# Kernel tuning notes

Hardware: AMD Instinct MI355X
Metric: run time of the kernel (lower is better)

The kernel has to match this reference:

```python
import jax, jax.numpy as jnp
import numpy as np

V, MAXLEN, D, I, C, L, S = 32000, 4096, 1024, 4096, 1024, 4, 4096


def setup_inputs() -> dict:
    key = jax.random.key(0)
    ks = jax.random.split(key, 20)
    sd = 0.02
    inp = {
        "input_indices": jax.random.randint(ks[0], (S,), 0, V),
        "emb": jax.random.normal(ks[1], (V, D), jnp.float32) * sd,
        "pos": jax.random.normal(ks[2], (MAXLEN, D), jnp.float32) * sd,
        "Wq": jax.random.normal(ks[3], (L, D, I), jnp.float32) * sd,
        "bq": jnp.zeros((L, I), jnp.float32),
        "Wk": jax.random.normal(ks[4], (L, D, I), jnp.float32) * sd,
        "bk": jnp.zeros((L, I), jnp.float32),
        "Wv": jax.random.normal(ks[5], (L, D, I), jnp.float32) * sd,
        "bv": jnp.zeros((L, I), jnp.float32),
        "Wo": jax.random.normal(ks[6], (L, I, D), jnp.float32) * sd,
        "bo": jnp.zeros((L, D), jnp.float32),
        "W1": jax.random.normal(ks[7], (L, D, I), jnp.float32) * sd,
        "b1": jnp.zeros((L, I), jnp.float32),
        "W2": jax.random.normal(ks[8], (L, I, D), jnp.float32) * sd,
        "b2": jnp.zeros((L, D), jnp.float32),
        "Wout": jax.random.normal(ks[9], (D, C), jnp.float32) * sd,
        "bout": jnp.zeros((C,), jnp.float32),
    }
    return inp


def reference(input_indices, emb, pos, Wq, bq, Wk, bk, Wv, bv, Wo, bo, W1, b1, W2, b2, Wout, bout):
    s = input_indices.shape[0]
    x = emb[input_indices] + pos[:s]  # [S, D]
    causal_mask = jnp.triu(jnp.ones((s, s), bool), k=1)  # True above diagonal -> masked
    scale = 1.0 / np.sqrt(Wq.shape[-1]).astype(np.float32)

    def layer(x, p):
        wq, bq_, wk, bk_, wv, bv_, wo, bo_, w1, b1_, w2, b2_ = p
        q = x @ wq + bq_  # [S, I]
        k = x @ wk + bk_
        v = x @ wv + bv_
        scores = (q @ k.T) * scale  # [S, S]
        scores = jnp.where(causal_mask, -jnp.inf, scores)
        attn = jax.nn.softmax(scores, axis=-1)
        r = x + (attn @ v) @ wo + bo_  # residual + attention output projection
        f = jnp.maximum(r @ w1 + b1_, 0.0) @ w2 + b2_  # ReLU FFN
        return r + f, attn

    x, attention_maps = jax.lax.scan(
        layer, x, (Wq, bq, Wk, bk, Wv, bv, Wo, bo, W1, b1, W2, b2)
    )
    logits = x @ Wout + bout  # [S, C]
    log_probs = jax.nn.log_softmax(logits, axis=-1)
    return log_probs, attention_maps  # [S, C], [L, S, S]
```

## Files before the change

kernel.cpp:

```cpp
#include <hip/hip_runtime.h>
#include <stdint.h>
#include <math.h>

#define S_ 4096
#define D_ 1024
#define I_ 4096
#define C_ 1024
#define L_ 4

typedef unsigned short u16;
typedef short bf16x8 __attribute__((ext_vector_type(8)));
typedef float f32x4 __attribute__((ext_vector_type(4)));

__device__ __forceinline__ u16 f2bf(float f) {
  union { float f; uint32_t u; } c; c.f = f;
  return (u16)((c.u + 0x7FFFu + ((c.u >> 16) & 1u)) >> 16);
}

__device__ __forceinline__ u16 f2h(float f) {
  _Float16 h = (_Float16)f;
  return *(u16*)&h;
}
__device__ __forceinline__ float h2f(u16 b) {
  _Float16 h = *(_Float16*)&b;
  return (float)h;
}

__device__ __forceinline__ void gll16(const void* g, void* l) {
  __builtin_amdgcn_global_load_lds(
      (__attribute__((address_space(1))) void*)(g),
      (__attribute__((address_space(3))) void*)(l), 16, 0, 0);
}

#define BAR() asm volatile("s_barrier" ::: "memory")
#define WAITV(n) asm volatile("s_waitcnt vmcnt(" #n ")" ::: "memory")

__device__ __forceinline__ int xcd_swz(int orig, int nwg) {
  int q8 = nwg >> 3, r8 = nwg & 7;
  int xcd = orig & 7, rem = orig >> 3;
  return (xcd < r8 ? xcd * (q8 + 1) : r8 * (q8 + 1) + (xcd - r8) * q8) + rem;
}

__device__ __forceinline__ void gemm256_body(
    u16* sA, u16* sB,
    const u16* __restrict__ A, const u16* __restrict__ Bt,
    const float* __restrict__ bias, const float* __restrict__ resid,
    float* __restrict__ outF, u16* __restrict__ outB, u16* __restrict__ outH,
    u16* __restrict__ outT, int ldT,
    int N, int K, float scale, int relu,
    int row0, int col0, int t0, int t1)
{
  int tid = threadIdx.x, l = tid & 63;
  int w = tid >> 6;
  int wr = w >> 2, wc = w & 3;
  int lrow = l & 15, lq = l >> 4;
  int hb = wc >> 1;
  int rx = lrow & 7;

  const u16* ap[2]; const u16* bp[2]; int dst[2];
#pragma unroll
  for (int u = 0; u < 2; ++u) {
    int c = u * 512 + tid;
    int row = c >> 3;
    int oct = (c & 7) ^ (row & 7);
    ap[u] = A + (size_t)(row0 + row) * K + oct * 8;
    bp[u] = Bt + (size_t)(col0 + row) * K + oct * 8;
    dst[u] = c * 8;
  }

#define STAGE_A(par, hh, t)                                                     \
  { _Pragma("unroll") for (int u = 0; u < 2; ++u)                               \
      gll16(ap[u] + (size_t)(hh) * 128 * K + (t) * 64,                          \
            &sA[((par) * 2 + (hh)) * 8192 + dst[u]]); }
#define STAGE_B(par, hh, t)                                                     \
  { _Pragma("unroll") for (int u = 0; u < 2; ++u)                               \
      gll16(bp[u] + (size_t)(hh) * 128 * K + (t) * 64,                          \
            &sB[((par) * 2 + (hh)) * 8192 + dst[u]]); }
#define LD_A(DST, par, mh)                                                      \
  { _Pragma("unroll") for (int mi = 0; mi < 4; ++mi)                            \
    _Pragma("unroll") for (int kc = 0; kc < 2; ++kc)                            \
      DST[mi][kc] = *(const bf16x8*)&sA[((par) * 2 + wr) * 8192 +               \
          ((mh) * 64 + mi * 16 + lrow) * 64 + (((kc * 4 + lq) ^ rx) * 8)]; }
#define LD_B(DST, par, nh)                                                      \
  { _Pragma("unroll") for (int nj = 0; nj < 2; ++nj)                            \
    _Pragma("unroll") for (int kc = 0; kc < 2; ++kc)                            \
      DST[nj][kc] = *(const bf16x8*)&sB[((par) * 2 + hb) * 8192 +               \
          ((wc & 1) * 64 + (nh) * 32 + nj * 16 + lrow) * 64 +                   \
          (((kc * 4 + lq) ^ rx) * 8)]; }

  f32x4 acc[8][4];
#pragma unroll
  for (int i = 0; i < 8; ++i)
#pragma unroll
    for (int j = 0; j < 4; ++j) {
      acc[i][j][0] = 0.f; acc[i][j][1] = 0.f; acc[i][j][2] = 0.f; acc[i][j][3] = 0.f;
    }

#define MM(AF, MB, NB)                                                          \
  { __builtin_amdgcn_s_setprio(1);                                             \
    _Pragma("unroll") for (int kc = 0; kc < 2; ++kc)                            \
    _Pragma("unroll") for (int mi = 0; mi < 4; ++mi)                            \
    _Pragma("unroll") for (int nj = 0; nj < 2; ++nj)                            \
      acc[(MB) + mi][(NB) + nj] = __builtin_amdgcn_mfma_f32_16x16x32_bf16(      \
          AF[mi][kc], bfv[nj][kc], acc[(MB) + mi][(NB) + nj], 0, 0, 0);         \
    __builtin_amdgcn_s_setprio(0); }

  bf16x8 afA[4][2], afB[4][2], bfv[2][2];

  STAGE_A(0, 0, t0); STAGE_A(0, 1, t0); STAGE_B(0, 0, t0); STAGE_B(0, 1, t0);
  STAGE_A(1, 0, t0 + 1); STAGE_A(1, 1, t0 + 1); STAGE_B(1, 0, t0 + 1);
  WAITV(6);
  BAR();

  for (int t = t0; t < t1; ++t) {
    int p = (t - t0) & 1;
    LD_A(afA, p, 0);
    LD_B(bfv, p, 0);
    LD_A(afB, p, 1);
    if (t + 1 < t1) STAGE_B(p ^ 1, 1, t + 1);
    BAR();
    MM(afA, 0, 0);
    BAR();
    if (t + 2 < t1) STAGE_A(p, 0, t + 2);
    BAR();
    MM(afB, 4, 0);
    BAR();
    LD_B(bfv, p, 1);
    if (t + 2 < t1) STAGE_A(p, 1, t + 2);
    BAR();
    MM(afB, 4, 2);
    BAR();
    if (t + 2 < t1) STAGE_B(p, 0, t + 2);
    BAR();
    MM(afA, 0, 2);
    if (t + 2 < t1) { WAITV(6); } else { WAITV(0); }
    BAR();
  }
#undef STAGE_A
#undef STAGE_B
#undef LD_A
#undef LD_B
#undef MM

  float biasv[4] = {0.f, 0.f, 0.f, 0.f};
  if (bias) {
#pragma unroll
    for (int j = 0; j < 4; ++j) biasv[j] = bias[col0 + wc * 64 + j * 16 + lrow];
  }

  if (outT) {
    u16* tlds = sA;
    int myhalf = wc >> 1;
    int colb = tid >> 5;
    int sub = tid & 31;
#pragma unroll
    for (int half = 0; half < 2; ++half) {
      BAR();
      if (myhalf == half) {
#pragma unroll
        for (int i = 0; i < 8; ++i)
#pragma unroll
          for (int r = 0; r < 4; ++r)
#pragma unroll
            for (int j = 0; j < 4; ++j) {
              int cl = (wc * 64 + j * 16 + lrow) & 127;
              int rowl = wr * 128 + i * 16 + lq * 4 + r;
              tlds[cl * 264 + rowl] = f2bf(acc[i][j][r] + biasv[j]);
            }
      }
      BAR();
#pragma unroll
      for (int it = 0; it < 8; ++it) {
        int cl = it * 16 + colb;
        size_t gb = (size_t)(col0 + half * 128 + cl) * ldT + row0 + sub * 8;
        bf16x8 v = *(const bf16x8*)&tlds[cl * 264 + sub * 8];
        *(bf16x8*)&outT[gb] = v;
      }
    }
    return;
  }

#pragma unroll
  for (int i = 0; i < 8; ++i) {
#pragma unroll
    for (int r = 0; r < 4; ++r) {
      int row = row0 + wr * 128 + i * 16 + lq * 4 + r;
      size_t ro = (size_t)row * N;
#pragma unroll
      for (int j = 0; j < 4; ++j) {
        int col = col0 + wc * 64 + j * 16 + lrow;
        float v = acc[i][j][r] * scale + biasv[j];
        if (resid) v += resid[ro + col];
        if (relu) v = fmaxf(v, 0.f);
        if (outF) outF[ro + col] = v;
        if (outB) outB[ro + col] = f2bf(v);
        if (outH) outH[ro + col] = f2h(v);
      }
    }
  }
}

__global__ __launch_bounds__(512, 2) void gemm256k(
    const u16* __restrict__ A, const u16* __restrict__ Bt,
    const float* __restrict__ bias, const float* __restrict__ resid,
    float* __restrict__ outF, u16* __restrict__ outB,
    int M, int N, int K, float scale, int flags, int k0, int k1)
{
  extern __shared__ char smem[];
  int wg = xcd_swz(blockIdx.x, gridDim.x);
  int nbx = N / 256;
  int br = wg / nbx, bc = wg % nbx;
  gemm256_body((u16*)smem, (u16*)smem + 32768, A, Bt, bias, resid, outF, outB,
               nullptr, nullptr, 0, N, K, scale, flags & 1, br * 256, bc * 256,
               k0 / 64, k1 / 64);
}

struct B3 { const float* b[3]; };
__global__ __launch_bounds__(512, 2) void gemm256_qkv(
    const u16* __restrict__ A, const u16* __restrict__ BtBase,
    B3 b3, u16* __restrict__ outQK, u16* __restrict__ vT, int K)
{
  extern __shared__ char smem[];
  int wg = xcd_swz(blockIdx.x, gridDim.x);
  int z = wg >> 8;
  int tile = wg & 255;
  int br = tile >> 4, bc = tile & 15;
  if (z < 2) {
    gemm256_body((u16*)smem, (u16*)smem + 32768, A,
                 BtBase + (size_t)z * I_ * D_, b3.b[z], nullptr,
                 nullptr, outQK + (size_t)z * S_ * I_, nullptr, nullptr, 0,
                 I_, K, 1.0f, 0, br * 256, bc * 256, 0, K / 64);
  } else {
    gemm256_body((u16*)smem, (u16*)smem + 32768, A,
                 BtBase + (size_t)2 * I_ * D_, b3.b[2], nullptr,
                 nullptr, nullptr, nullptr, vT, S_,
                 I_, K, 1.0f, 0, br * 256, bc * 256, 0, K / 64);
  }
}

__global__ __launch_bounds__(512, 2) void gemm256_tri3(
    const u16* __restrict__ A, const u16* __restrict__ Bt,
    u16* __restrict__ out0, u16* __restrict__ out1, u16* __restrict__ out2,
    int K, float scale)
{
  extern __shared__ char smem[];
  int wg = xcd_swz(blockIdx.x, gridDim.x);
  int ntri = gridDim.x / 3;
  int chunk = wg / ntri;
  int tile = wg - chunk * ntri;
  int br = (int)((sqrtf(8.0f * (float)tile + 1.0f) - 1.0f) * 0.5f);
  while ((br + 1) * (br + 2) / 2 <= tile) ++br;
  while (br * (br + 1) / 2 > tile) --br;
  int bc = tile - br * (br + 1) / 2;
  int t0 = (chunk == 0) ? 0 : (chunk == 1 ? 22 : 43);
  int t1 = (chunk == 0) ? 22 : (chunk == 1 ? 43 : 64);
  u16* o = (chunk == 0) ? out0 : (chunk == 1 ? out1 : out2);
  gemm256_body((u16*)smem, (u16*)smem + 32768, A, Bt, nullptr, nullptr,
               nullptr, nullptr, o, nullptr, 0,
               S_, K, scale, 0, br * 256, bc * 256, t0, t1);
}

__global__ __launch_bounds__(512, 2) void gemm256_pv(
    const u16* __restrict__ A, const u16* __restrict__ Bt,
    u16* __restrict__ outB, u16* __restrict__ pvH)
{
  extern __shared__ char smem[];
  int wg = xcd_swz(blockIdx.x, gridDim.x);
  if (wg < 128) {
    int br = wg >> 4, bc = wg & 15;
    gemm256_body((u16*)smem, (u16*)smem + 32768, A, Bt, nullptr, nullptr,
                 nullptr, outB, nullptr, nullptr, 0, I_, S_, 1.0f, 0,
                 br * 256, bc * 256, 0, (br + 1) * 4);
  } else {
    int c = wg - 128;
    int br = 8 + (c >> 5);
    int bc = (c >> 1) & 15;
    int chunk = c & 1;
    int lim = (br + 1) * 4;
    int half = lim >> 1;
    u16* o = pvH + (size_t)chunk * (S_ / 2) * I_ - (size_t)2048 * I_;
    gemm256_body((u16*)smem, (u16*)smem + 32768, A, Bt, nullptr, nullptr,
                 nullptr, nullptr, o, nullptr, 0, I_, S_, 1.0f, 0,
                 br * 256, bc * 256, chunk ? half : 0, chunk ? lim : half);
  }
}

__global__ __launch_bounds__(256) void combine2pv(
    const u16* __restrict__ pvH, u16* __restrict__ outB)
{
  const int MN = (S_ / 2) * I_;
  int i = (blockIdx.x * 256 + threadIdx.x) * 4;
  ushort4 a = *(const ushort4*)&pvH[i];
  ushort4 b = *(const ushort4*)&pvH[MN + i];
  ushort4 o;
  o.x = f2bf(h2f(a.x) + h2f(b.x));
  o.y = f2bf(h2f(a.y) + h2f(b.y));
  o.z = f2bf(h2f(a.z) + h2f(b.z));
  o.w = f2bf(h2f(a.w) + h2f(b.w));
  *(ushort4*)&outB[(size_t)2048 * I_ + i] = o;
}

__global__ __launch_bounds__(512, 2) void gemm256_ks4(
    const u16* __restrict__ A, const u16* __restrict__ Bt,
    u16* __restrict__ pOut, int M, int N, int K)
{
  extern __shared__ char smem[];
  int wg = xcd_swz(blockIdx.x, gridDim.x);
  int chunk = wg & 3;
  int tile = wg >> 2;
  int nbx = N / 256;
  int br = tile / nbx, bc = tile % nbx;
  u16* o = pOut + (size_t)chunk * M * N;
  int kq = K / 4;
  gemm256_body((u16*)smem, (u16*)smem + 32768, A, Bt, nullptr, nullptr,
               nullptr, nullptr, o, nullptr, 0, N, K, 1.0f, 0,
               br * 256, bc * 256, (chunk * kq) / 64, ((chunk + 1) * kq) / 64);
}

__global__ __launch_bounds__(256) void combine4(
    const u16* __restrict__ p, const float* __restrict__ bias,
    const float* __restrict__ resid, float* __restrict__ outF,
    u16* __restrict__ outB, int MN, int N)
{
  int i = (blockIdx.x * 256 + threadIdx.x) * 4;
  ushort4 a = *(const ushort4*)&p[i];
  ushort4 b = *(const ushort4*)&p[MN + i];
  ushort4 c = *(const ushort4*)&p[2 * MN + i];
  ushort4 d = *(const ushort4*)&p[3 * MN + i];
  f32x4 v;
  v[0] = h2f(a.x) + h2f(b.x) + h2f(c.x) + h2f(d.x);
  v[1] = h2f(a.y) + h2f(b.y) + h2f(c.y) + h2f(d.y);
  v[2] = h2f(a.z) + h2f(b.z) + h2f(c.z) + h2f(d.z);
  v[3] = h2f(a.w) + h2f(b.w) + h2f(c.w) + h2f(d.w);
  int col = i & (N - 1);
  v += *(const f32x4*)&bias[col];
  v += *(const f32x4*)&resid[i];
  *(f32x4*)&outF[i] = v;
  ushort4 o;
  o.x = f2bf(v[0]); o.y = f2bf(v[1]); o.z = f2bf(v[2]); o.w = f2bf(v[3]);
  *(ushort4*)&outB[i] = o;
}

template <int BM_, int BN_>
__global__ __launch_bounds__(256) void gemm_bt(
    const u16* __restrict__ A, const u16* __restrict__ Bt,
    const float* __restrict__ bias, const float* __restrict__ resid,
    float* __restrict__ outF, u16* __restrict__ outB,
    int M, int N, int K, float scale, int flags)
{
  constexpr int FM = BM_ / 32;
  constexpr int FN = BN_ / 32;
  constexpr int ALOADS = BM_ * 8 / 256;
  constexpr int BLOADS = BN_ * 8 / 256;
  constexpr int WROWS = BM_ / 2;
  constexpr int WCOLS = BN_ / 2;

  int wg = xcd_swz(blockIdx.x, gridDim.x);
  int nbx = N / BN_;
  int br = wg / nbx, bc = wg % nbx;

  int tid = threadIdx.x;
  int l = tid & 63, w = tid >> 6;
  int wr = w >> 1, wc = w & 1;
  int lrow = l & 15, lq = l >> 4;
  int row0 = br * BM_, col0 = bc * BN_;

  __shared__ u16 lA[2][BM_ * 64];
  __shared__ u16 lB[2][BN_ * 64];

  const u16* aptr[ALOADS];
  const u16* bptr[BLOADS];
#pragma unroll
  for (int t = 0; t < ALOADS; ++t) {
    int c = t * 256 + tid;
    int row = c >> 3;
    int oct = (c & 7) ^ (row & 7);
    aptr[t] = A + (size_t)(row0 + row) * K + oct * 8;
  }
#pragma unroll
  for (int t = 0; t < BLOADS; ++t) {
    int c = t * 256 + tid;
    int row = c >> 3;
    int oct = (c & 7) ^ (row & 7);
    bptr[t] = Bt + (size_t)(col0 + row) * K + oct * 8;
  }

#define STAGE(b, koff)                                                          \
  {                                                                             \
    _Pragma("unroll") for (int t = 0; t < ALOADS; ++t)                          \
        gll16(aptr[t] + (koff), &lA[b][(t * 256 + tid) * 8]);                   \
    _Pragma("unroll") for (int t = 0; t < BLOADS; ++t)                          \
        gll16(bptr[t] + (koff), &lB[b][(t * 256 + tid) * 8]);                   \
  }

  f32x4 acc[FM][FN];
#pragma unroll
  for (int i = 0; i < FM; ++i)
#pragma unroll
    for (int j = 0; j < FN; ++j) {
      acc[i][j][0] = 0.f; acc[i][j][1] = 0.f; acc[i][j][2] = 0.f; acc[i][j][3] = 0.f;
    }

  int ktiles = K / 64;
  int rxA = lrow & 7;

  STAGE(0, 0);
  __syncthreads();
  int cur = 0;
  for (int kt = 0; kt < ktiles; ++kt) {
    if (kt + 1 < ktiles) STAGE(cur ^ 1, (kt + 1) * 64);
#pragma unroll
    for (int kc = 0; kc < 2; ++kc) {
      int kq = kc * 4 + lq;
      int octA = (kq ^ rxA) * 8;
      bf16x8 af[FM], bfv[FN];
#pragma unroll
      for (int i = 0; i < FM; ++i)
        af[i] = *(const bf16x8*)&lA[cur][(wr * WROWS + i * 16 + lrow) * 64 + octA];
#pragma unroll
      for (int j = 0; j < FN; ++j)
        bfv[j] = *(const bf16x8*)&lB[cur][(wc * WCOLS + j * 16 + lrow) * 64 + octA];
#pragma unroll
      for (int i = 0; i < FM; ++i)
#pragma unroll
        for (int j = 0; j < FN; ++j)
          acc[i][j] = __builtin_amdgcn_mfma_f32_16x16x32_bf16(af[i], bfv[j], acc[i][j], 0, 0, 0);
    }
    __syncthreads();
    cur ^= 1;
  }
#undef STAGE

  float biasv[FN];
#pragma unroll
  for (int j = 0; j < FN; ++j) biasv[j] = 0.f;
  if (bias) {
#pragma unroll
    for (int j = 0; j < FN; ++j) biasv[j] = bias[col0 + wc * WCOLS + j * 16 + lrow];
  }
  bool do_relu = (flags & 1) != 0;
#pragma unroll
  for (int i = 0; i < FM; ++i) {
#pragma unroll
    for (int r = 0; r < 4; ++r) {
      int row = row0 + wr * WROWS + i * 16 + lq * 4 + r;
      size_t ro = (size_t)row * N;
#pragma unroll
      for (int j = 0; j < FN; ++j) {
        int col = col0 + wc * WCOLS + j * 16 + lrow;
        float v = acc[i][j][r] * scale + biasv[j];
        if (resid) v += resid[ro + col];
        if (do_relu) v = fmaxf(v, 0.f);
        if (outF) outF[ro + col] = v;
        if (outB) outB[ro + col] = f2bf(v);
      }
    }
  }
}

struct T6 {
  const float* src[6];
  u16* dst[6];
};

__global__ __launch_bounds__(256) void trans6_f2b(T6 a) {
  __shared__ float tile[64][65];
  int z = blockIdx.z;
  bool big = (z == 3 || z == 5);
  int R = big ? I_ : D_;
  int C = big ? D_ : I_;
  int bid = blockIdx.y * gridDim.x + blockIdx.x;
  int nbx = C / 64;
  int bx = bid % nbx, by = bid / nbx;
  const float* src = a.src[z];
  u16* dst = a.dst[z];
  int c0 = bx * 64, r0 = by * 64;
  int tx = threadIdx.x & 63, ty = threadIdx.x >> 6;
#pragma unroll
  for (int i = 0; i < 64; i += 4)
    tile[ty + i][tx] = src[(size_t)(r0 + ty + i) * C + c0 + tx];
  __syncthreads();
#pragma unroll
  for (int i = 0; i < 64; i += 4)
    dst[(size_t)(c0 + ty + i) * R + r0 + tx] = f2bf(tile[tx][ty + i]);
}

__global__ __launch_bounds__(256) void trans_f2b(const float* __restrict__ src,
                                                 u16* __restrict__ dst, int R, int C)
{
  __shared__ float tile[32][33];
  int c0 = blockIdx.x * 32, r0 = blockIdx.y * 32;
  int tx = threadIdx.x & 31, ty = threadIdx.x >> 5;
#pragma unroll
  for (int i = 0; i < 32; i += 8)
    tile[ty + i][tx] = src[(size_t)(r0 + ty + i) * C + c0 + tx];
  __syncthreads();
#pragma unroll
  for (int i = 0; i < 32; i += 8)
    dst[(size_t)(c0 + ty + i) * R + r0 + tx] = f2bf(tile[tx][ty + i]);
}

__global__ __launch_bounds__(256) void embed_k(const int* __restrict__ idx,
                                               const float* __restrict__ emb,
                                               const float* __restrict__ pos,
                                               float* __restrict__ xf, u16* __restrict__ xb)
{
  int i = (blockIdx.x * 256 + threadIdx.x) * 8;
  int s = i >> 10;
  int d = i & (D_ - 1);
  const float* e = emb + (size_t)idx[s] * D_ + d;
  const float* p = pos + (size_t)s * D_ + d;
  f32x4 v0 = *(const f32x4*)e + *(const f32x4*)p;
  f32x4 v1 = *(const f32x4*)(e + 4) + *(const f32x4*)(p + 4);
  *(f32x4*)&xf[i] = v0;
  *(f32x4*)&xf[i + 4] = v1;
  ushort4 b0, b1;
  b0.x = f2bf(v0[0]); b0.y = f2bf(v0[1]); b0.z = f2bf(v0[2]); b0.w = f2bf(v0[3]);
  b1.x = f2bf(v1[0]); b1.y = f2bf(v1[1]); b1.z = f2bf(v1[2]); b1.w = f2bf(v1[3]);
  *(ushort4*)&xb[i] = b0;
  *(ushort4*)&xb[i + 4] = b1;
}

__global__ __launch_bounds__(256) void softmax_causal(float* __restrict__ att,
                                                      const u16* __restrict__ p0,
                                                      const u16* __restrict__ p1,
                                                      const u16* __restrict__ p2,
                                                      u16* __restrict__ attB)
{
  int s = blockIdx.x;
  __shared__ float row[S_];
  __shared__ float red[8];
  int tid = threadIdx.x, l = tid & 63, w = tid >> 6;
  int nv = s + 1;
  size_t base = (size_t)s * S_;
  float m = -3.0e38f;
  for (int c = tid; c < nv; c += 256) {
    float v = h2f(p0[base + c]) + h2f(p1[base + c]) + h2f(p2[base + c]);
    row[c] = v; m = fmaxf(m, v);
  }
#pragma unroll
  for (int off = 32; off; off >>= 1) m = fmaxf(m, __shfl_xor(m, off, 64));
  if (l == 0) red[w] = m;
  __syncthreads();
  m = fmaxf(fmaxf(red[0], red[1]), fmaxf(red[2], red[3]));
  float sum = 0.f;
  for (int c = tid; c < nv; c += 256) { float e = __expf(row[c] - m); row[c] = e; sum += e; }
#pragma unroll
  for (int off = 32; off; off >>= 1) sum += __shfl_xor(sum, off, 64);
  if (l == 0) red[4 + w] = sum;
  __syncthreads();
  sum = red[4] + red[5] + red[6] + red[7];
  float inv = 1.0f / sum;
  int nb = ((s >> 8) + 1) * 256;
  for (int c = tid; c < S_; c += 256) {
    float p = (c < nv) ? row[c] * inv : 0.0f;
    att[base + c] = p;
    if (c < nb) attB[base + c] = f2bf(p);
  }
}

__global__ __launch_bounds__(256) void logsoftmax_k(const float* __restrict__ logits,
                                                    float* __restrict__ out)
{
  int s = blockIdx.x;
  int tid = threadIdx.x, l = tid & 63, w = tid >> 6;
  __shared__ float red[8];
  size_t base = (size_t)s * C_;
  float v[4];
  float m = -3.0e38f;
#pragma unroll
  for (int k = 0; k < 4; ++k) { v[k] = logits[base + tid + k * 256]; m = fmaxf(m, v[k]); }
#pragma unroll
  for (int off = 32; off; off >>= 1) m = fmaxf(m, __shfl_xor(m, off, 64));
  if (l == 0) red[w] = m;
  __syncthreads();
  m = fmaxf(fmaxf(red[0], red[1]), fmaxf(red[2], red[3]));
  float sum = 0.f;
#pragma unroll
  for (int k = 0; k < 4; ++k) sum += __expf(v[k] - m);
#pragma unroll
  for (int off = 32; off; off >>= 1) sum += __shfl_xor(sum, off, 64);
  if (l == 0) red[4 + w] = sum;
  __syncthreads();
  sum = red[4] + red[5] + red[6] + red[7];
  float lz = logf(sum);
#pragma unroll
  for (int k = 0; k < 4; ++k) out[base + tid + k * 256] = v[k] - m - lz;
}

extern "C" void kernel_launch(void* const* d_in, const int* in_sizes, int n_in,
                              void* d_out, int out_size, void* d_ws, size_t ws_size,
                              hipStream_t stream) {
  (void)in_sizes; (void)n_in; (void)out_size; (void)ws_size;
  const int*   idx  = (const int*)d_in[0];
  const float* emb  = (const float*)d_in[1];
  const float* pos  = (const float*)d_in[2];
  const float* Wq   = (const float*)d_in[3];
  const float* bq   = (const float*)d_in[4];
  const float* Wk   = (const float*)d_in[5];
  const float* bk   = (const float*)d_in[6];
  const float* Wv   = (const float*)d_in[7];
  const float* bv   = (const float*)d_in[8];
  const float* Wo   = (const float*)d_in[9];
  const float* bo   = (const float*)d_in[10];
  const float* W1   = (const float*)d_in[11];
  const float* b1   = (const float*)d_in[12];
  const float* W2   = (const float*)d_in[13];
  const float* b2   = (const float*)d_in[14];
  const float* Wout = (const float*)d_in[15];
  const float* bout = (const float*)d_in[16];
  float* out = (float*)d_out;

  char* ws = (char*)d_ws;
  const size_t MB = 1024ull * 1024ull;
  float* xres  = (float*)(ws + 0);
  u16*  xbf    = (u16*)(ws + 16 * MB);
  u16*  bufQ   = (u16*)(ws + 24 * MB);
  u16*  bufK   = (u16*)(ws + 56 * MB);
  u16*  bufVT  = (u16*)(ws + 120 * MB);
  u16*  attnB  = (u16*)(ws + 152 * MB);
  float* logit = (float*)(ws + 184 * MB);
  u16* WqT   = (u16*)(ws + 200 * MB);
  u16* WkT   = (u16*)(ws + 208 * MB);
  u16* WvT   = (u16*)(ws + 216 * MB);
  u16* WoT   = (u16*)(ws + 224 * MB);
  u16* W1T   = (u16*)(ws + 232 * MB);
  u16* W2T   = (u16*)(ws + 240 * MB);
  u16* WoutT = (u16*)(ws + 248 * MB);
  u16* attP0 = (u16*)(ws + 256 * MB);
  u16* attP1 = (u16*)(ws + 288 * MB);
  u16* attP2 = (u16*)(ws + 320 * MB);
  u16* shP   = (u16*)(ws + 352 * MB);

  const float iscale = 1.0f / 64.0f;
  const int LDSB = 131072;
  hipFuncSetAttribute((const void*)gemm256k,
                      hipFuncAttributeMaxDynamicSharedMemorySize, LDSB);
  hipFuncSetAttribute((const void*)gemm256_qkv,
                      hipFuncAttributeMaxDynamicSharedMemorySize, LDSB);
  hipFuncSetAttribute((const void*)gemm256_tri3,
                      hipFuncAttributeMaxDynamicSharedMemorySize, LDSB);
  hipFuncSetAttribute((const void*)gemm256_pv,
                      hipFuncAttributeMaxDynamicSharedMemorySize, LDSB);
  hipFuncSetAttribute((const void*)gemm256_ks4,
                      hipFuncAttributeMaxDynamicSharedMemorySize, LDSB);
  const int G_SQ = (S_ / 256) * (I_ / 256);

  embed_k<<<(S_ * D_) / (256 * 8), 256, 0, stream>>>(idx, emb, pos, xres, xbf);

  for (int layer = 0; layer < L_; ++layer) {
    T6 t6;
    t6.src[0] = Wq + (size_t)layer * D_ * I_; t6.dst[0] = WqT;
    t6.src[1] = Wk + (size_t)layer * D_ * I_; t6.dst[1] = WkT;
    t6.src[2] = Wv + (size_t)layer * D_ * I_; t6.dst[2] = WvT;
    t6.src[3] = Wo + (size_t)layer * I_ * D_; t6.dst[3] = WoT;
    t6.src[4] = W1 + (size_t)layer * D_ * I_; t6.dst[4] = W1T;
    t6.src[5] = W2 + (size_t)layer * I_ * D_; t6.dst[5] = W2T;
    trans6_f2b<<<dim3(64, 16, 6), 256, 0, stream>>>(t6);

    B3 b3;
    b3.b[0] = bq + (size_t)layer * I_;
    b3.b[1] = bk + (size_t)layer * I_;
    b3.b[2] = bv + (size_t)layer * I_;
    gemm256_qkv<<<3 * G_SQ, 512, LDSB, stream>>>(xbf, WqT, b3, bufQ, bufVT, D_);

    float* attL = out + (size_t)S_ * C_ + (size_t)layer * S_ * S_;
    gemm256_tri3<<<3 * 136, 512, LDSB, stream>>>(bufQ, bufK, attP0, attP1, attP2,
                                                 I_, iscale);

    softmax_causal<<<S_, 256, 0, stream>>>(attL, attP0, attP1, attP2, attnB);

    gemm256_pv<<<384, 512, LDSB, stream>>>(attnB, bufVT, bufQ, shP);
    combine2pv<<<(S_ / 2) * (I_ / 1024), 256, 0, stream>>>(shP, bufQ);

    gemm256_ks4<<<(S_ / 256) * (D_ / 256) * 4, 512, LDSB, stream>>>(
        bufQ, WoT, shP, S_, D_, I_);
    combine4<<<(S_ * D_) / 1024, 256, 0, stream>>>(
        shP, bo + (size_t)layer * D_, xres, xres, xbf, S_ * D_, D_);

    gemm256k<<<G_SQ, 512, LDSB, stream>>>(
        xbf, W1T, b1 + (size_t)layer * I_, nullptr, nullptr, bufK,
        S_, I_, D_, 1.0f, 1, 0, D_);

    gemm256_ks4<<<(S_ / 256) * (D_ / 256) * 4, 512, LDSB, stream>>>(
        bufK, W2T, shP, S_, D_, I_);
    combine4<<<(S_ * D_) / 1024, 256, 0, stream>>>(
        shP, b2 + (size_t)layer * D_, xres, xres, xbf, S_ * D_, D_);
  }

  trans_f2b<<<dim3(C_ / 32, D_ / 32), 256, 0, stream>>>(Wout, WoutT, D_, C_);
  gemm_bt<64, 128><<<(S_ / 64) * (C_ / 128), 256, 0, stream>>>(
      xbf, WoutT, bout, nullptr, logit, nullptr, S_, C_, D_, 1.0f, 0);
  logsoftmax_k<<<S_, 256, 0, stream>>>(logit, out);
}
```

Baseline: 2.140 ms.

## Keep residual stream in bf16 only and use split-K GEMM for output logits

Drops the fp32 residual buffer, so embedding and combine kernels read and write only the bf16 copy, which cuts memory traffic in the combine passes. The final classifier GEMM switches from a small-tile gemm_bt to the 256-tile split-K kernel, and the partial-sum combine plus bias is fused into the log-softmax kernel. In exchange the residual accumulates in bf16 across layers, which loses precision, and the partials are stored in fp16.

```diff
diff --git a/kernel.cpp b/kernel.cpp
--- a/kernel.cpp
+++ b/kernel.cpp
@@ -16,7 +16,10 @@
   union { float f; uint32_t u; } c; c.f = f;
   return (u16)((c.u + 0x7FFFu + ((c.u >> 16) & 1u)) >> 16);
 }
-
+__device__ __forceinline__ float bf2f(u16 b) {
+  union { uint32_t u; float f; } c; c.u = (uint32_t)b << 16;
+  return c.f;
+}
 __device__ __forceinline__ u16 f2h(float f) {
   _Float16 h = (_Float16)f;
   return *(u16*)&h;
@@ -319,143 +322,24 @@
 
 __global__ __launch_bounds__(256) void combine4(
     const u16* __restrict__ p, const float* __restrict__ bias,
-    const float* __restrict__ resid, float* __restrict__ outF,
-    u16* __restrict__ outB, int MN, int N)
+    const u16* __restrict__ residB, u16* __restrict__ outB, int MN, int N)
 {
   int i = (blockIdx.x * 256 + threadIdx.x) * 4;
   ushort4 a = *(const ushort4*)&p[i];
   ushort4 b = *(const ushort4*)&p[MN + i];
   ushort4 c = *(const ushort4*)&p[2 * MN + i];
   ushort4 d = *(const ushort4*)&p[3 * MN + i];
+  ushort4 rb = *(const ushort4*)&residB[i];
   f32x4 v;
-  v[0] = h2f(a.x) + h2f(b.x) + h2f(c.x) + h2f(d.x);
-  v[1] = h2f(a.y) + h2f(b.y) + h2f(c.y) + h2f(d.y);
-  v[2] = h2f(a.z) + h2f(b.z) + h2f(c.z) + h2f(d.z);
-  v[3] = h2f(a.w) + h2f(b.w) + h2f(c.w) + h2f(d.w);
+  v[0] = h2f(a.x) + h2f(b.x) + h2f(c.x) + h2f(d.x) + bf2f(rb.x);
+  v[1] = h2f(a.y) + h2f(b.y) + h2f(c.y) + h2f(d.y) + bf2f(rb.y);
+  v[2] = h2f(a.z) + h2f(b.z) + h2f(c.z) + h2f(d.z) + bf2f(rb.z);
+  v[3] = h2f(a.w) + h2f(b.w) + h2f(c.w) + h2f(d.w) + bf2f(rb.w);
   int col = i & (N - 1);
   v += *(const f32x4*)&bias[col];
-  v += *(const f32x4*)&resid[i];
-  *(f32x4*)&outF[i] = v;
   ushort4 o;
   o.x = f2bf(v[0]); o.y = f2bf(v[1]); o.z = f2bf(v[2]); o.w = f2bf(v[3]);
   *(ushort4*)&outB[i] = o;
-}
-
-template <int BM_, int BN_>
-__global__ __launch_bounds__(256) void gemm_bt(
-    const u16* __restrict__ A, const u16* __restrict__ Bt,
-    const float* __restrict__ bias, const float* __restrict__ resid,
-    float* __restrict__ outF, u16* __restrict__ outB,
-    int M, int N, int K, float scale, int flags)
-{
-  constexpr int FM = BM_ / 32;
-  constexpr int FN = BN_ / 32;
-  constexpr int ALOADS = BM_ * 8 / 256;
-  constexpr int BLOADS = BN_ * 8 / 256;
-  constexpr int WROWS = BM_ / 2;
-  constexpr int WCOLS = BN_ / 2;
-
-  int wg = xcd_swz(blockIdx.x, gridDim.x);
-  int nbx = N / BN_;
-  int br = wg / nbx, bc = wg % nbx;
-
-  int tid = threadIdx.x;
-  int l = tid & 63, w = tid >> 6;
-  int wr = w >> 1, wc = w & 1;
-  int lrow = l & 15, lq = l >> 4;
-  int row0 = br * BM_, col0 = bc * BN_;
-
-  __shared__ u16 lA[2][BM_ * 64];
-  __shared__ u16 lB[2][BN_ * 64];
-
-  const u16* aptr[ALOADS];
-  const u16* bptr[BLOADS];
-#pragma unroll
-  for (int t = 0; t < ALOADS; ++t) {
-    int c = t * 256 + tid;
-    int row = c >> 3;
-    int oct = (c & 7) ^ (row & 7);
-    aptr[t] = A + (size_t)(row0 + row) * K + oct * 8;
-  }
-#pragma unroll
-  for (int t = 0; t < BLOADS; ++t) {
-    int c = t * 256 + tid;
-    int row = c >> 3;
-    int oct = (c & 7) ^ (row & 7);
-    bptr[t] = Bt + (size_t)(col0 + row) * K + oct * 8;
-  }
-
-#define STAGE(b, koff)                                                          \
-  {                                                                             \
-    _Pragma("unroll") for (int t = 0; t < ALOADS; ++t)                          \
-        gll16(aptr[t] + (koff), &lA[b][(t * 256 + tid) * 8]);                   \
-    _Pragma("unroll") for (int t = 0; t < BLOADS; ++t)                          \
-        gll16(bptr[t] + (koff), &lB[b][(t * 256 + tid) * 8]);                   \
-  }
-
-  f32x4 acc[FM][FN];
-#pragma unroll
-  for (int i = 0; i < FM; ++i)
-#pragma unroll
-    for (int j = 0; j < FN; ++j) {
-      acc[i][j][0] = 0.f; acc[i][j][1] = 0.f; acc[i][j][2] = 0.f; acc[i][j][3] = 0.f;
-    }
-
-  int ktiles = K / 64;
-  int rxA = lrow & 7;
-
-  STAGE(0, 0);
-  __syncthreads();
-  int cur = 0;
-  for (int kt = 0; kt < ktiles; ++kt) {
-    if (kt + 1 < ktiles) STAGE(cur ^ 1, (kt + 1) * 64);
-#pragma unroll
-    for (int kc = 0; kc < 2; ++kc) {
-      int kq = kc * 4 + lq;
-      int octA = (kq ^ rxA) * 8;
-      bf16x8 af[FM], bfv[FN];
-#pragma unroll
-      for (int i = 0; i < FM; ++i)
-        af[i] = *(const bf16x8*)&lA[cur][(wr * WROWS + i * 16 + lrow) * 64 + octA];
-#pragma unroll
-      for (int j = 0; j < FN; ++j)
-        bfv[j] = *(const bf16x8*)&lB[cur][(wc * WCOLS + j * 16 + lrow) * 64 + octA];
-#pragma unroll
-      for (int i = 0; i < FM; ++i)
-#pragma unroll
-        for (int j = 0; j < FN; ++j)
-          acc[i][j] = __builtin_amdgcn_mfma_f32_16x16x32_bf16(af[i], bfv[j], acc[i][j], 0, 0, 0);
-    }
-    __syncthreads();
-    cur ^= 1;
-  }
-#undef STAGE
-
-  float biasv[FN];
-#pragma unroll
-  for (int j = 0; j < FN; ++j) biasv[j] = 0.f;
-  if (bias) {
-#pragma unroll
-    for (int j = 0; j < FN; ++j) biasv[j] = bias[col0 + wc * WCOLS + j * 16 + lrow];
-  }
-  bool do_relu = (flags & 1) != 0;
-#pragma unroll
-  for (int i = 0; i < FM; ++i) {
-#pragma unroll
-    for (int r = 0; r < 4; ++r) {
-      int row = row0 + wr * WROWS + i * 16 + lq * 4 + r;
-      size_t ro = (size_t)row * N;
-#pragma unroll
-      for (int j = 0; j < FN; ++j) {
-        int col = col0 + wc * WCOLS + j * 16 + lrow;
-        float v = acc[i][j][r] * scale + biasv[j];
-        if (resid) v += resid[ro + col];
-        if (do_relu) v = fmaxf(v, 0.f);
-        if (outF) outF[ro + col] = v;
-        if (outB) outB[ro + col] = f2bf(v);
-      }
-    }
-  }
 }
 
 struct T6 {
@@ -503,7 +387,7 @@
 __global__ __launch_bounds__(256) void embed_k(const int* __restrict__ idx,
                                                const float* __restrict__ emb,
                                                const float* __restrict__ pos,
-                                               float* __restrict__ xf, u16* __restrict__ xb)
+                                               u16* __restrict__ xb)
 {
   int i = (blockIdx.x * 256 + threadIdx.x) * 8;
   int s = i >> 10;
@@ -512,8 +396,6 @@
   const float* p = pos + (size_t)s * D_ + d;
   f32x4 v0 = *(const f32x4*)e + *(const f32x4*)p;
   f32x4 v1 = *(const f32x4*)(e + 4) + *(const f32x4*)(p + 4);
-  *(f32x4*)&xf[i] = v0;
-  *(f32x4*)&xf[i + 4] = v1;
   ushort4 b0, b1;
   b0.x = f2bf(v0[0]); b0.y = f2bf(v0[1]); b0.z = f2bf(v0[2]); b0.w = f2bf(v0[3]);
   b1.x = f2bf(v1[0]); b1.y = f2bf(v1[1]); b1.z = f2bf(v1[2]); b1.w = f2bf(v1[3]);
@@ -559,9 +441,11 @@
   }
 }
 
-__global__ __launch_bounds__(256) void logsoftmax_k(const float* __restrict__ logits,
+__global__ __launch_bounds__(256) void logsoftmax_k(const u16* __restrict__ p,
+                                                    const float* __restrict__ bias,
                                                     float* __restrict__ out)
 {
+  const int MN = S_ * C_;
   int s = blockIdx.x;
   int tid = threadIdx.x, l = tid & 63, w = tid >> 6;
   __shared__ float red[8];
@@ -569,7 +453,13 @@
   float v[4];
   float m = -3.0e38f;
 #pragma unroll
-  for (int k = 0; k < 4; ++k) { v[k] = logits[base + tid + k * 256]; m = fmaxf(m, v[k]); }
+  for (int k = 0; k < 4; ++k) {
+    int col = tid + k * 256;
+    size_t i = base + col;
+    v[k] = h2f(p[i]) + h2f(p[MN + i]) + h2f(p[2 * MN + i]) + h2f(p[3 * MN + i])
+           + bias[col];
+    m = fmaxf(m, v[k]);
+  }
 #pragma unroll
   for (int off = 32; off; off >>= 1) m = fmaxf(m, __shfl_xor(m, off, 64));
   if (l == 0) red[w] = m;
@@ -613,13 +503,11 @@
 
   char* ws = (char*)d_ws;
   const size_t MB = 1024ull * 1024ull;
-  float* xres  = (float*)(ws + 0);
   u16*  xbf    = (u16*)(ws + 16 * MB);
   u16*  bufQ   = (u16*)(ws + 24 * MB);
   u16*  bufK   = (u16*)(ws + 56 * MB);
   u16*  bufVT  = (u16*)(ws + 120 * MB);
   u16*  attnB  = (u16*)(ws + 152 * MB);
-  float* logit = (float*)(ws + 184 * MB);
   u16* WqT   = (u16*)(ws + 200 * MB);
   u16* WkT   = (u16*)(ws + 208 * MB);
   u16* WvT   = (u16*)(ws + 216 * MB);
@@ -646,7 +534,7 @@
                       hipFuncAttributeMaxDynamicSharedMemorySize, LDSB);
   const int G_SQ = (S_ / 256) * (I_ / 256);
 
-  embed_k<<<(S_ * D_) / (256 * 8), 256, 0, stream>>>(idx, emb, pos, xres, xbf);
+  embed_k<<<(S_ * D_) / (256 * 8), 256, 0, stream>>>(idx, emb, pos, xbf);
 
   for (int layer = 0; layer < L_; ++layer) {
     T6 t6;
@@ -676,7 +564,7 @@
     gemm256_ks4<<<(S_ / 256) * (D_ / 256) * 4, 512, LDSB, stream>>>(
         bufQ, WoT, shP, S_, D_, I_);
     combine4<<<(S_ * D_) / 1024, 256, 0, stream>>>(
-        shP, bo + (size_t)layer * D_, xres, xres, xbf, S_ * D_, D_);
+        shP, bo + (size_t)layer * D_, xbf, xbf, S_ * D_, D_);
 
     gemm256k<<<G_SQ, 512, LDSB, stream>>>(
         xbf, W1T, b1 + (size_t)layer * I_, nullptr, nullptr, bufK,
@@ -685,11 +573,11 @@
     gemm256_ks4<<<(S_ / 256) * (D_ / 256) * 4, 512, LDSB, stream>>>(
         bufK, W2T, shP, S_, D_, I_);
     combine4<<<(S_ * D_) / 1024, 256, 0, stream>>>(
-        shP, b2 + (size_t)layer * D_, xres, xres, xbf, S_ * D_, D_);
+        shP, b2 + (size_t)layer * D_, xbf, xbf, S_ * D_, D_);
   }
 
   trans_f2b<<<dim3(C_ / 32, D_ / 32), 256, 0, stream>>>(Wout, WoutT, D_, C_);
-  gemm_bt<64, 128><<<(S_ / 64) * (C_ / 128), 256, 0, stream>>>(
-      xbf, WoutT, bout, nullptr, logit, nullptr, S_, C_, D_, 1.0f, 0);
-  logsoftmax_k<<<S_, 256, 0, stream>>>(logit, out);
-}
+  gemm256_ks4<<<(S_ / 256) * (C_ / 256) * 4, 512, LDSB, stream>>>(
+      xbf, WoutT, shP, S_, C_, D_);
+  logsoftmax_k<<<S_, 256, 0, stream>>>(shP, bout, out);
+}
```

Result: no change. 2.100 ms (-1.9%).
